# Kernel tuning notes

Measured on AMD Instinct MI355X. Metric: run time of the kernel, lower is better.

## Reference

```python
import math
import jax, jax.numpy as jnp
import numpy as np

B, T, D_MODEL, H = 2, 2048, 1024, 16
D_HEAD = D_MODEL // H
EPS = 1e-9


def setup_inputs() -> dict:
    key = jax.random.key(0)
    ks = jax.random.split(key, 5)
    std = 1.0 / math.sqrt(D_MODEL)
    return {
        "x": jax.random.normal(ks[0], (B, T, D_MODEL), dtype=jnp.float32),
        "Wq": jax.random.normal(ks[1], (D_MODEL, D_MODEL), dtype=jnp.float32) * std,
        "Wk": jax.random.normal(ks[2], (D_MODEL, D_MODEL), dtype=jnp.float32) * std,
        "Wv": jax.random.normal(ks[3], (D_MODEL, D_MODEL), dtype=jnp.float32) * std,
        "Wo": jax.random.normal(ks[4], (D_MODEL, D_MODEL), dtype=jnp.float32) * std,
    }


def _attention(x, Wq, Wk, Wv, Wo):
    b, t, d = x.shape
    # projections (nn.Linear without bias: y = x @ W^T)
    q = (x @ Wq.T).reshape(b, t, H, D_HEAD).transpose(0, 2, 1, 3)  # (B,H,T,dh)
    k = (x @ Wk.T).reshape(b, t, H, D_HEAD).transpose(0, 2, 1, 3)
    v = (x @ Wv.T).reshape(b, t, H, D_HEAD).transpose(0, 2, 1, 3)
    scale = 1.0 / math.sqrt(D_HEAD)
    scores = jnp.einsum("bhqd,bhkd->bhqk", q, k) * scale  # (B,H,T,T)
    causal = jnp.tril(jnp.ones((t, t), dtype=bool))
    scores = jnp.where(causal[None, None], scores, -jnp.inf)
    # stable softmax with +eps in denominator (matches online-softmax accumulation)
    m = jnp.max(scores, axis=-1, keepdims=True)
    e = jnp.exp(scores - m)
    l = jnp.sum(e, axis=-1, keepdims=True)
    attn_out = jnp.einsum("bhqk,bhkd->bhqd", e, v) / (l + EPS)
    out = attn_out.transpose(0, 2, 1, 3).reshape(b, t, d)
    return out @ Wo.T


def reference(x, Wq, Wk, Wv, Wo):
    return _attention(x, Wq, Wk, Wv, Wo)
```

## Files before the change

### kernel.cpp

```cpp
#include <hip/hip_runtime.h>
#include <hip/hip_bf16.h>


typedef __attribute__((ext_vector_type(8))) short bf16x8;
typedef __attribute__((ext_vector_type(4))) short short4v;
typedef __attribute__((ext_vector_type(4))) float f32x4;

#define T_SEQ 2048
#define D_MODEL 1024
#define NHEAD 16
#define DHEAD 64
#define QK_SCALE 0.180336879f

__device__ inline short f2bf(float f) {
    unsigned u = __float_as_uint(f);
    u += 0x7fffu + ((u >> 16) & 1u);
    return (short)(u >> 16);
}

__device__ inline unsigned pk2(float a, float b) {
    __hip_bfloat162 h = __float22bfloat162_rn(make_float2(a, b));
    return *(unsigned*)&h;
}

__device__ inline unsigned long long pk4(float a, float b, float c, float d) {
    return (unsigned long long)pk2(a, b) | ((unsigned long long)pk2(c, d) << 32);
}

__device__ inline f32x4 mfma16(bf16x8 a, bf16x8 b, f32x4 c) {
    return __builtin_amdgcn_mfma_f32_16x16x32_bf16(a, b, c, 0, 0, 0);
}

__device__ inline void gld_lds16(const short* g, short* l) {
    __builtin_amdgcn_global_load_lds(
        (const __attribute__((address_space(1))) void*)g,
        (__attribute__((address_space(3))) void*)l, 16, 0, 0);
}

__global__ __launch_bounds__(256) void cast_all(const float* __restrict__ x,
                                                const float* __restrict__ w0,
                                                const float* __restrict__ w1,
                                                const float* __restrict__ w2,
                                                const float* __restrict__ w3,
                                                short* __restrict__ xdst,
                                                short* __restrict__ wdst) {
    int i = (blockIdx.x * 256 + threadIdx.x) * 4;
    const float* s;
    short* d;
    if (blockIdx.y == 0) {
        s = x + i; d = xdst + i;
    } else {
        int m = i >> 20;
        s = ((m == 0) ? w0 : (m == 1) ? w1 : (m == 2) ? w2 : w3) + (i & 1048575);
        d = wdst + i;
    }
    float4 v = *(const float4*)s;
    short4v o = { f2bf(v.x), f2bf(v.y), f2bf(v.z), f2bf(v.w) };
    *(short4v*)d = o;
}

__global__ __launch_bounds__(256, 3) void gemm_qkv(const short* __restrict__ A,
                                                   const short* __restrict__ B,
                                                   short* __restrict__ C0,
                                                   short* __restrict__ C1,
                                                   short* __restrict__ C2,
                                                   int M, int N, int K) {
    __shared__ short As[4096];
    __shared__ short Bs[4096];

    const int tid = threadIdx.x;
    const int wave = tid >> 6, lane = tid & 63;
    const int g = lane >> 4, ln = lane & 15;
    const int mh = wave & 1, nh = wave >> 1;
    const int m_base = blockIdx.x * 128;
    const int n_base = blockIdx.y * 128;
    const int swz8 = 8 * (g ^ ((ln >> 1) & 3));

    const int srow = tid >> 2;
    const int scol = (((tid & 3) ^ ((tid >> 3) & 3))) * 8;
    const short* Ag = A + (long)(m_base + srow) * K + scol;
    const short* Bg = B + (long)(n_base + srow) * K + scol;
    const long r64 = 64 * (long)K;

    f32x4 acc[4][4];
#pragma unroll
    for (int i = 0; i < 4; i++)
#pragma unroll
        for (int j = 0; j < 4; j++) acc[i][j] = (f32x4){0.f, 0.f, 0.f, 0.f};

    for (int k0 = 0; k0 < K; k0 += 32) {
        gld_lds16(Ag + k0, As + tid * 8);
        gld_lds16(Ag + r64 + k0, As + 2048 + tid * 8);
        gld_lds16(Bg + k0, Bs + tid * 8);
        gld_lds16(Bg + r64 + k0, Bs + 2048 + tid * 8);
        __syncthreads();

        bf16x8 a[4], b[4];
#pragma unroll
        for (int mf = 0; mf < 4; mf++)
            a[mf] = *(const bf16x8*)(As + (mh * 64 + mf * 16 + ln) * 32 + swz8);
#pragma unroll
        for (int nf = 0; nf < 4; nf++)
            b[nf] = *(const bf16x8*)(Bs + (nh * 64 + nf * 16 + ln) * 32 + swz8);
#pragma unroll
        for (int mf = 0; mf < 4; mf++)
#pragma unroll
            for (int nf = 0; nf < 4; nf++)
                acc[mf][nf] = mfma16(a[mf], b[nf], acc[mf][nf]);
        __syncthreads();
    }

    const int mat = n_base >> 10;
    if (mat < 2) {
        short* dst = mat == 0 ? C0 : C1;
        const float scl = (mat == 0) ? QK_SCALE : 1.f;
#pragma unroll
        for (int mf = 0; mf < 4; mf++)
#pragma unroll
            for (int nf = 0; nf < 4; nf++)
#pragma unroll
                for (int r = 0; r < 4; r++) {
                    int row = m_base + mh * 64 + mf * 16 + g * 4 + r;
                    int cc = (n_base & 1023) + nh * 64 + nf * 16 + ln;
                    int b_ = row >> 11, t = row & 2047;
                    int h = cc >> 6, d = cc & 63;
                    dst[(((long)(b_ * NHEAD + h) * T_SEQ + t) << 6) + d] =
                        f2bf(acc[mf][nf][r] * scl);
                }
    } else {
        short* dst = C2;
#pragma unroll
        for (int mf = 0; mf < 4; mf++)
#pragma unroll
            for (int nf = 0; nf < 4; nf++) {
                unsigned long long pk = pk4(acc[mf][nf][0], acc[mf][nf][1],
                                            acc[mf][nf][2], acc[mf][nf][3]);
                int cc = (n_base & 1023) + nh * 64 + nf * 16 + ln;
                int row0 = m_base + mh * 64 + mf * 16 + g * 4;
                int b_ = row0 >> 11, t = row0 & 2047;
                *(unsigned long long*)(&dst[((long)(b_ * 1024 + cc) << 11) + t]) = pk;
            }
    }
}

__global__ __launch_bounds__(256, 3) void gemm_out(const short* __restrict__ A,
                                                   const short* __restrict__ B,
                                                   float* __restrict__ C,
                                                   int M, int N, int K) {
    __shared__ short As[4096];
    __shared__ short Bs[2048];

    const int tid = threadIdx.x;
    const int wave = tid >> 6, lane = tid & 63;
    const int g = lane >> 4, ln = lane & 15;
    const int mh = wave & 1, nh = wave >> 1;
    const int m_base = blockIdx.x * 128;
    const int n_base = blockIdx.y * 64;
    const int swz8 = 8 * (g ^ ((ln >> 1) & 3));

    const int srow = tid >> 2;
    const int scol = (((tid & 3) ^ ((tid >> 3) & 3))) * 8;
    const short* Ag = A + (long)(m_base + srow) * K + scol;
    const short* Bg = B + (long)(n_base + srow) * K + scol;
    const long r64 = 64 * (long)K;

    f32x4 acc[4][2];
#pragma unroll
    for (int i = 0; i < 4; i++)
#pragma unroll
        for (int j = 0; j < 2; j++) acc[i][j] = (f32x4){0.f, 0.f, 0.f, 0.f};

    for (int k0 = 0; k0 < K; k0 += 32) {
        gld_lds16(Ag + k0, As + tid * 8);
        gld_lds16(Ag + r64 + k0, As + 2048 + tid * 8);
        gld_lds16(Bg + k0, Bs + tid * 8);
        __syncthreads();

        bf16x8 a[4], b[2];
#pragma unroll
        for (int mf = 0; mf < 4; mf++)
            a[mf] = *(const bf16x8*)(As + (mh * 64 + mf * 16 + ln) * 32 + swz8);
#pragma unroll
        for (int nf = 0; nf < 2; nf++)
            b[nf] = *(const bf16x8*)(Bs + (nh * 32 + nf * 16 + ln) * 32 + swz8);
#pragma unroll
        for (int mf = 0; mf < 4; mf++)
#pragma unroll
            for (int nf = 0; nf < 2; nf++)
                acc[mf][nf] = mfma16(a[mf], b[nf], acc[mf][nf]);
        __syncthreads();
    }

#pragma unroll
    for (int mf = 0; mf < 4; mf++)
#pragma unroll
        for (int nf = 0; nf < 2; nf++)
#pragma unroll
            for (int r = 0; r < 4; r++) {
                int row = m_base + mh * 64 + mf * 16 + g * 4 + r;
                int col = n_base + nh * 32 + nf * 16 + ln;
                C[(long)row * N + col] = acc[mf][nf][r];
            }
}

__global__ __launch_bounds__(256) void flash_attn(const short* __restrict__ Q,
                                                  const short* __restrict__ Kx,
                                                  const short* __restrict__ Vt,
                                                  short* __restrict__ O) {
    __shared__ short Ks[2][4096];
    __shared__ short Vs[2][4096];
    __shared__ short ldsP[4][16][68];

    const int tid = threadIdx.x;
    const int wv = tid >> 6, lane = tid & 63;
    const int g = lane >> 4, ln = lane & 15;
    const int id = blockIdx.x;
    const int qx = 31 - (id >> 5);
    const int bh = id & 31;
    const int swz8 = 8 * (g ^ ((ln >> 1) & 3));

    const short* Kp = Kx + (long)bh * (T_SEQ * DHEAD);
    const short* Vp = Vt + (long)bh * (DHEAD * T_SEQ);

    const int sr = tid >> 2;
    const int sc8 = (((tid & 3) ^ ((tid >> 3) & 3))) * 8;
    const int offK0 = sr * 64 + sc8;
    const long offV0 = (long)sr * T_SEQ + sc8;
    const int ldst = tid * 8;

    const int nt = qx + 1;
    const int qrow0 = qx * 64 + wv * 16;

    const short* Qp = Q + ((long)bh * T_SEQ + qrow0) * DHEAD;
    bf16x8 qf0 = *(const bf16x8*)(Qp + ln * 64 + 8 * g);
    bf16x8 qf1 = *(const bf16x8*)(Qp + ln * 64 + 32 + 8 * g);

    f32x4 o[4];
#pragma unroll
    for (int nf = 0; nf < 4; nf++) o[nf] = (f32x4){0.f, 0.f, 0.f, 0.f};
    float li = 0.f;

    gld_lds16(Kp + offK0, &Ks[0][ldst]);
    gld_lds16(Kp + offK0 + 32, &Ks[0][2048 + ldst]);
    gld_lds16(Vp + offV0, &Vs[0][ldst]);
    gld_lds16(Vp + offV0 + 32, &Vs[0][2048 + ldst]);

    int buf = 0;
    for (int i = 0; i < nt; i++) {
        __syncthreads();
        if (i + 1 < nt) {
            const int kO = (i + 1) * 4096 + offK0;
            const long vO = offV0 + (i + 1) * 64;
            gld_lds16(Kp + kO, &Ks[buf ^ 1][ldst]);
            gld_lds16(Kp + kO + 32, &Ks[buf ^ 1][2048 + ldst]);
            gld_lds16(Vp + vO, &Vs[buf ^ 1][ldst]);
            gld_lds16(Vp + vO + 32, &Vs[buf ^ 1][2048 + ldst]);
        }

        f32x4 s[4];
#pragma unroll
        for (int j = 0; j < 4; j++) {
            bf16x8 k0 = *(const bf16x8*)(&Ks[buf][(j * 16 + ln) * 32 + swz8]);
            bf16x8 k1 = *(const bf16x8*)(&Ks[buf][2048 + (j * 16 + ln) * 32 + swz8]);
            s[j] = mfma16(k0, qf0, (f32x4){0.f, 0.f, 0.f, 0.f});
            s[j] = mfma16(k1, qf1, s[j]);
        }

        bf16x8 vf[4][2];
#pragma unroll
        for (int nf = 0; nf < 4; nf++) {
            vf[nf][0] = *(const bf16x8*)(&Vs[buf][(nf * 16 + ln) * 32 + swz8]);
            vf[nf][1] = *(const bf16x8*)(&Vs[buf][2048 + (nf * 16 + ln) * 32 + swz8]);
        }

        if (i == nt - 1) {
            const int ql = 16 * wv + ln;
#pragma unroll
            for (int j = 0; j < 4; j++) {
                int kl = 16 * j + 4 * g;
#pragma unroll
                for (int r = 0; r < 4; r++)
                    if (kl + r > ql) s[j][r] = -INFINITY;
            }
        }

#pragma unroll
        for (int j = 0; j < 4; j++) {
            float e0 = __builtin_amdgcn_exp2f(s[j][0]);
            float e1 = __builtin_amdgcn_exp2f(s[j][1]);
            float e2 = __builtin_amdgcn_exp2f(s[j][2]);
            float e3 = __builtin_amdgcn_exp2f(s[j][3]);
            li += (e0 + e1) + (e2 + e3);
            *(unsigned long long*)(&ldsP[wv][ln][16 * j + 4 * g]) =
                pk4(e0, e1, e2, e3);
        }

        asm volatile("s_waitcnt lgkmcnt(0)" ::: "memory");
        bf16x8 pa0 = *(const bf16x8*)(&ldsP[wv][ln][8 * g]);
        bf16x8 pa1 = *(const bf16x8*)(&ldsP[wv][ln][32 + 8 * g]);

#pragma unroll
        for (int nf = 0; nf < 4; nf++) {
            o[nf] = mfma16(pa0, vf[nf][0], o[nf]);
            o[nf] = mfma16(pa1, vf[nf][1], o[nf]);
        }
        buf ^= 1;
    }

    li += __shfl_xor(li, 16);
    li += __shfl_xor(li, 32);

    float lr[4];
#pragma unroll
    for (int r = 0; r < 4; r++)
        lr[r] = 1.f / (__shfl(li, 4 * g + r) + 1e-9f);

    const int b = bh >> 4, h = bh & 15;
#pragma unroll
    for (int nf = 0; nf < 4; nf++) {
#pragma unroll
        for (int r = 0; r < 4; r++) {
            int rr = qrow0 + g * 4 + r;
            O[((long)(b * T_SEQ + rr) << 10) + h * 64 + nf * 16 + ln] =
                f2bf(o[nf][r] * lr[r]);
        }
    }
}

extern "C" void kernel_launch(void* const* d_in, const int* in_sizes, int n_in,
                              void* d_out, int out_size, void* d_ws, size_t ws_size,
                              hipStream_t stream) {
    const float* x  = (const float*)d_in[0];
    const float* Wq = (const float*)d_in[1];
    const float* Wk = (const float*)d_in[2];
    const float* Wv = (const float*)d_in[3];
    const float* Wo = (const float*)d_in[4];

    char* ws = (char*)d_ws;
    short* xb  = (short*)(ws + (0ull  << 20));
    short* wqb = (short*)(ws + (8ull  << 20));
    short* wob = (short*)(ws + (14ull << 20));
    short* Qb  = (short*)(ws + (16ull << 20));
    short* Kb  = (short*)(ws + (24ull << 20));
    short* Vtb = (short*)(ws + (32ull << 20));
    short* Ab  = (short*)(ws + (40ull << 20));

    cast_all<<<dim3(4096, 2), 256, 0, stream>>>(x, Wq, Wk, Wv, Wo, xb, wqb);

    gemm_qkv<<<dim3(32, 24), 256, 0, stream>>>(xb, wqb, Qb, Kb, Vtb,
                                               4096, 3072, 1024);

    flash_attn<<<1024, 256, 0, stream>>>(Qb, Kb, Vtb, Ab);

    gemm_out<<<dim3(32, 16), 256, 0, stream>>>(Ab, wob, (float*)d_out,
                                               4096, 1024, 1024);
}
```

Before: 168.5 us.

## Feed P directly from registers via 16x16x16 MFMA, drop LDS P round-trip

Replaces the per-wave LDS staging of the softmax probabilities P with a direct register path. P's S-accumulator layout now serves as the A operand of 16x16x16 bf16 MFMAs. V tiles are loaded with a new XOR swizzle over 64-wide rows so each lane reads 4-element fragments matching that layout. This removes an LDS write, a waitcnt stall and two LDS reads per tile. In exchange it issues twice as many smaller MFMAs (16 vs 8 per tile) and sixteen 8-byte V reads instead of eight 16-byte ones.

```diff
diff --git a/kernel.cpp b/kernel.cpp
--- a/kernel.cpp
+++ b/kernel.cpp
@@ -29,6 +29,10 @@
 
 __device__ inline f32x4 mfma16(bf16x8 a, bf16x8 b, f32x4 c) {
     return __builtin_amdgcn_mfma_f32_16x16x32_bf16(a, b, c, 0, 0, 0);
+}
+
+__device__ inline f32x4 mfma1616(short4v a, short4v b, f32x4 c) {
+    return __builtin_amdgcn_mfma_f32_16x16x16bf16_1k(a, b, c, 0, 0, 0);
 }
 
 __device__ inline void gld_lds16(const short* g, short* l) {
@@ -209,7 +213,6 @@
                                                   short* __restrict__ O) {
     __shared__ short Ks[2][4096];
     __shared__ short Vs[2][4096];
-    __shared__ short ldsP[4][16][68];
 
     const int tid = threadIdx.x;
     const int wv = tid >> 6, lane = tid & 63;
@@ -225,7 +228,9 @@
     const int sr = tid >> 2;
     const int sc8 = (((tid & 3) ^ ((tid >> 3) & 3))) * 8;
     const int offK0 = sr * 64 + sc8;
-    const long offV0 = (long)sr * T_SEQ + sc8;
+    const int vd0 = tid >> 3, vd1 = (256 + tid) >> 3;
+    const long offV0 = (long)vd0 * T_SEQ + 8 * ((tid & 7) ^ ((vd0 >> 1) & 7));
+    const long offV1 = (long)vd1 * T_SEQ + 8 * ((tid & 7) ^ ((vd1 >> 1) & 7));
     const int ldst = tid * 8;
 
     const int nt = qx + 1;
@@ -243,18 +248,25 @@
     gld_lds16(Kp + offK0, &Ks[0][ldst]);
     gld_lds16(Kp + offK0 + 32, &Ks[0][2048 + ldst]);
     gld_lds16(Vp + offV0, &Vs[0][ldst]);
-    gld_lds16(Vp + offV0 + 32, &Vs[0][2048 + ldst]);
+    gld_lds16(Vp + offV1, &Vs[0][2048 + ldst]);
+
+    int voff[4][4];
+#pragma unroll
+    for (int j = 0; j < 4; j++)
+#pragma unroll
+        for (int nf = 0; nf < 4; nf++)
+            voff[j][nf] = (nf * 16 + ln) * 64 +
+                          8 * ((2 * j + (g >> 1)) ^ ((ln >> 1) & 7)) + 4 * (g & 1);
 
     int buf = 0;
     for (int i = 0; i < nt; i++) {
         __syncthreads();
         if (i + 1 < nt) {
             const int kO = (i + 1) * 4096 + offK0;
-            const long vO = offV0 + (i + 1) * 64;
             gld_lds16(Kp + kO, &Ks[buf ^ 1][ldst]);
             gld_lds16(Kp + kO + 32, &Ks[buf ^ 1][2048 + ldst]);
-            gld_lds16(Vp + vO, &Vs[buf ^ 1][ldst]);
-            gld_lds16(Vp + vO + 32, &Vs[buf ^ 1][2048 + ldst]);
+            gld_lds16(Vp + offV0 + (i + 1) * 64, &Vs[buf ^ 1][ldst]);
+            gld_lds16(Vp + offV1 + (i + 1) * 64, &Vs[buf ^ 1][2048 + ldst]);
         }
 
         f32x4 s[4];
@@ -266,12 +278,12 @@
             s[j] = mfma16(k1, qf1, s[j]);
         }
 
-        bf16x8 vf[4][2];
-#pragma unroll
-        for (int nf = 0; nf < 4; nf++) {
-            vf[nf][0] = *(const bf16x8*)(&Vs[buf][(nf * 16 + ln) * 32 + swz8]);
-            vf[nf][1] = *(const bf16x8*)(&Vs[buf][2048 + (nf * 16 + ln) * 32 + swz8]);
-        }
+        short4v vv[4][4];
+#pragma unroll
+        for (int j = 0; j < 4; j++)
+#pragma unroll
+            for (int nf = 0; nf < 4; nf++)
+                vv[j][nf] = *(const short4v*)(&Vs[buf][voff[j][nf]]);
 
         if (i == nt - 1) {
             const int ql = 16 * wv + ln;
@@ -291,18 +303,11 @@
             float e2 = __builtin_amdgcn_exp2f(s[j][2]);
             float e3 = __builtin_amdgcn_exp2f(s[j][3]);
             li += (e0 + e1) + (e2 + e3);
-            *(unsigned long long*)(&ldsP[wv][ln][16 * j + 4 * g]) =
-                pk4(e0, e1, e2, e3);
-        }
-
-        asm volatile("s_waitcnt lgkmcnt(0)" ::: "memory");
-        bf16x8 pa0 = *(const bf16x8*)(&ldsP[wv][ln][8 * g]);
-        bf16x8 pa1 = *(const bf16x8*)(&ldsP[wv][ln][32 + 8 * g]);
-
-#pragma unroll
-        for (int nf = 0; nf < 4; nf++) {
-            o[nf] = mfma16(pa0, vf[nf][0], o[nf]);
-            o[nf] = mfma16(pa1, vf[nf][1], o[nf]);
+            unsigned long long p = pk4(e0, e1, e2, e3);
+            short4v pa = *(short4v*)&p;
+#pragma unroll
+            for (int nf = 0; nf < 4; nf++)
+                o[nf] = mfma1616(pa, vv[j][nf], o[nf]);
         }
         buf ^= 1;
     }
```

Result: no change. 169.5 us (+0.6%).
